# Performance work log

Hardware: AMD Instinct MI355X
Metric: run time of the kernel (lower is better)

## Reference

```python
import jax, jax.numpy as jnp
import numpy as np

N, D, B, E = 3072, 64, 12, 49152


def _gat_conv(x, mask, W, a_src, a_dst, b):
    # PyG GATConv (eval mode): per-edge score = LeakyReLU(a_dst.Wx_i + a_src.Wx_j),
    # softmax over incoming neighbors (mask includes self-loops), concat heads.
    H, d = a_src.shape
    h = (x @ W).reshape(x.shape[0], H, d)                  # [N, H, d]
    es = jnp.einsum('nhd,hd->nh', h, a_src)                # source-side score
    ed = jnp.einsum('nhd,hd->nh', h, a_dst)                # dest-side score
    e = jax.nn.leaky_relu(ed[:, None, :] + es[None, :, :], 0.2)  # [Ndst, Nsrc, H]
    e = jnp.where(mask[:, :, None], e, -jnp.inf)
    alpha = jax.nn.softmax(e, axis=1)                      # softmax over sources
    out = jnp.einsum('ijh,jhd->ihd', alpha, h)
    return out.reshape(x.shape[0], H * d) + b


def _gcn_conv(x, Abool, W, b):
    # PyG GCNConv: add self-loops, symmetric deg^{-1/2} normalization.
    n = x.shape[0]
    Ahat = Abool.astype(x.dtype) + jnp.eye(n, dtype=x.dtype)
    deg = Ahat.sum(1)
    dinv = jnp.where(deg > 0, 1.0 / jnp.sqrt(deg), 0.0)
    return (dinv[:, None] * Ahat * dinv[None, :]) @ (x @ W) + b


def _forward(x, ei, g1_W, g1_as, g1_ad, g1_b, g2_W, g2_as, g2_ad, g2_b,
             gA_W, gA_b, gB_W, gB_b, gC_W, gC_b, c2_W, c2_b, c3_W, c3_b,
             hwA_W, hwA_b, hwB_W, hwB_b, gru_Wih, gru_Whh, gru_bih, gru_bhh,
             tA_W, tA_b, tB_W, tB_b, edge_index, atom_list, res_list):
    n = x.shape[0]
    relu = jax.nn.relu
    I = jnp.eye(n, dtype=bool)
    # A[dst, src] = 1 (PyG messages flow src -> dst); ei only sets to_dense_adj
    # values in the original, which are never used (only adj.shape).
    A = jnp.zeros((n, n), dtype=bool).at[edge_index[1], edge_index[0]].set(True)
    Af = A.astype(x.dtype)
    A2 = (Af @ Af) > 0                      # spspmm(E, E): 2-hop edges
    A3 = (Af @ A2.astype(x.dtype)) > 0      # spspmm(E^2, E): 3-hop edges
    counts = atom_list + res_list
    batch = jnp.repeat(jnp.arange(counts.shape[0]), counts, total_repeat_length=n)

    def gat_block(mask):
        v = jax.nn.elu(_gat_conv(x, mask, g1_W, g1_as, g1_ad, g1_b))
        v = relu(_gat_conv(v, mask, g2_W, g2_as, g2_ad, g2_b))
        v = relu(v @ gA_W + gA_b)
        v = relu(v @ gB_W + gB_b)
        return v @ gC_W + gC_b

    h1 = relu(gat_block(A | I))
    h1 = relu(_gcn_conv(h1, A, c2_W, c2_b))
    h1 = relu(_gcn_conv(h1, A, c3_W, c3_b))          # [N, 4D]
    h2 = relu(gat_block(A2 | I))
    h2 = relu(_gcn_conv(h2, A2, c2_W, c2_b))          # [N, 2D]
    h3 = relu(gat_block(A3 | I))                      # [N, D]
    # HighWay fusion
    bb = h2 @ hwB_W + hwB_b
    aa = h1 @ hwA_W + hwA_b
    z = jax.nn.sigmoid(aa + bb)
    hh = z * bb + (1.0 - z) * aa
    # GRUCell(input=h3, hidden=hh), PyTorch gate order r, z, n
    gx = h3 @ gru_Wih + gru_bih
    gh = hh @ gru_Whh + gru_bhh
    xr, xz, xn = jnp.split(gx, 3, axis=1)
    hr, hz, hn = jnp.split(gh, 3, axis=1)
    r = jax.nn.sigmoid(xr + hr)
    zz = jax.nn.sigmoid(xz + hz)
    nn_ = jnp.tanh(xn + r * hn)
    cc = (1.0 - zz) * nn_ + zz * hh
    vi = jax.ops.segment_max(cc, batch, num_segments=atom_list.shape[0])  # global_max_pool
    vi = relu(vi @ tA_W + tA_b)
    return vi @ tB_W + tB_b


def setup_inputs() -> dict:
    key = jax.random.key(0)
    ks = jax.random.split(key, 40)
    it = iter(range(40))

    def p(shp):
        return jax.random.normal(ks[next(it)], shp, dtype=jnp.float32) * 0.1

    src = jax.random.randint(ks[next(it)], (E,), 0, N)
    dst = jax.random.randint(ks[next(it)], (E,), 0, N)
    dst = jnp.where(dst == src, (dst + 1) % N, dst)   # no self-loops in raw edges
    edge_index = jnp.stack([src, dst])
    inp = {
        'x': jax.random.normal(ks[next(it)], (N, D), dtype=jnp.float32),
        'ei': jax.random.uniform(ks[next(it)], (E,), dtype=jnp.float32),
        'g1_W': p((D, 8 * D)), 'g1_as': p((8, D)), 'g1_ad': p((8, D)), 'g1_b': p((8 * D,)),
        'g2_W': p((8 * D, D)), 'g2_as': p((1, D)), 'g2_ad': p((1, D)), 'g2_b': p((D,)),
        'gA_W': p((D, D)), 'gA_b': p((D,)), 'gB_W': p((D, 128)), 'gB_b': p((128,)),
        'gC_W': p((128, D)), 'gC_b': p((D,)),
        'c2_W': p((D, 2 * D)), 'c2_b': p((2 * D,)), 'c3_W': p((2 * D, 4 * D)), 'c3_b': p((4 * D,)),
        'hwA_W': p((4 * D, D)), 'hwA_b': p((D,)), 'hwB_W': p((2 * D, D)), 'hwB_b': p((D,)),
        'gru_Wih': p((D, 3 * D)), 'gru_Whh': p((D, 3 * D)), 'gru_bih': p((3 * D,)), 'gru_bhh': p((3 * D,)),
        'tA_W': p((D, 128)), 'tA_b': p((128,)), 'tB_W': p((128, 120)), 'tB_b': p((120,)),
        'edge_index': edge_index,
        'atom_list': jnp.full((B,), 156, dtype=jnp.int32),
        'res_list': jnp.full((B,), 100, dtype=jnp.int32),
    }
    return inp


def reference(x, ei, g1_W, g1_as, g1_ad, g1_b, g2_W, g2_as, g2_ad, g2_b,
              gA_W, gA_b, gB_W, gB_b, gC_W, gC_b, c2_W, c2_b, c3_W, c3_b,
              hwA_W, hwA_b, hwB_W, hwB_b, gru_Wih, gru_Whh, gru_bih, gru_bhh,
              tA_W, tA_b, tB_W, tB_b, edge_index, atom_list, res_list):
    return _forward(x, ei, g1_W, g1_as, g1_ad, g1_b, g2_W, g2_as, g2_ad, g2_b,
                    gA_W, gA_b, gB_W, gB_b, gC_W, gC_b, c2_W, c2_b, c3_W, c3_b,
                    hwA_W, hwA_b, hwB_W, hwB_b, gru_Wih, gru_Whh, gru_bih, gru_bhh,
                    tA_W, tA_b, tB_W, tB_b, edge_index, atom_list, res_list)
```

## Files before the change

### kernel.cpp

```cpp
#include <hip/hip_runtime.h>
#include <math.h>

namespace {

constexpr int NN = 3072;
constexpr int NW = 96;
constexpr int NEDGE_C = 49152;
constexpr int NB = 12;

using short8v = __attribute__((ext_vector_type(8))) short;
using f32x4v  = __attribute__((ext_vector_type(4))) float;
typedef unsigned short ushort_t;

__device__ __forceinline__ float leaky02(float x) { return x > 0.f ? x : 0.2f * x; }
__device__ __forceinline__ float sigm(float x) { return 1.f / (1.f + __expf(-x)); }

__device__ __forceinline__ ushort_t f2bf(float x) {
  unsigned u = __float_as_uint(x);
  return (ushort_t)((u + 0x7fffu + ((u >> 16) & 1u)) >> 16);
}
__device__ __forceinline__ float bf2f(ushort_t b) {
  return __uint_as_float(((unsigned)b) << 16);
}
__device__ __forceinline__ unsigned pack_h(float a, float b) {
  return (unsigned)f2bf(a) | ((unsigned)f2bf(b) << 16);
}
__device__ __forceinline__ unsigned pack_l(float a, float b) {
  float ra = a - bf2f(f2bf(a));
  float rb = b - bf2f(f2bf(b));
  return (unsigned)f2bf(ra) | ((unsigned)f2bf(rb) << 16);
}

template<int ACT> __device__ __forceinline__ float act_apply(float v) {
  if (ACT == 1) return fmaxf(v, 0.f);
  if (ACT == 2) return v > 0.f ? v : (__expf(v) - 1.f);
  return v;
}

__global__ __launch_bounds__(256) void k_scatter(const int* __restrict__ ei,
                                                 unsigned* __restrict__ bits) {
  int e = blockIdx.x * 256 + threadIdx.x;
  if (e < NEDGE_C) {
    int s = ei[e];
    int d = ei[NEDGE_C + e];
    atomicOr(&bits[(size_t)d * NW + (s >> 5)], 1u << (s & 31));
  }
}

__global__ __launch_bounds__(128) void k_bmm(const unsigned* __restrict__ a,
                                             const unsigned* __restrict__ src2,
                                             unsigned* __restrict__ outb) {
  __shared__ unsigned row[NW];
  int d = blockIdx.x;
  int t = threadIdx.x;
  if (t < NW) row[t] = a[(size_t)d * NW + t];
  __syncthreads();
  unsigned acc = 0;
  for (int w = 0; w < NW; ++w) {
    unsigned m = row[w];
    while (m) {
      int b = __ffs(m) - 1; m &= m - 1;
      int k = w * 32 + b;
      if (t < NW) acc |= src2[(size_t)k * NW + t];
    }
  }
  if (t < NW) outb[(size_t)d * NW + t] = acc;
}

__global__ __launch_bounds__(256) void k_dinv(const unsigned* __restrict__ bits,
                                              float* __restrict__ dinv) {
  int i = blockIdx.x * 256 + threadIdx.x;
  if (i < NN) {
    int c = 0;
    for (int w = 0; w < NW; ++w) c += __popc(bits[(size_t)i * NW + w]);
    dinv[i] = 1.0f / sqrtf((float)(c + 1));
  }
}

template<int ACT>
__global__ __launch_bounds__(256) void k_gemm(const float* __restrict__ X,
                                              const float* __restrict__ Wm,
                                              const float* __restrict__ bias,
                                              float* __restrict__ Y,
                                              int K, int Nc) {
  __shared__ float Xt[32][68];
  __shared__ float Wt[32][68];
  int R0 = blockIdx.x * 64, C0 = blockIdx.y * 64;
  int t = threadIdx.x;
  int rg = t >> 4, dg = t & 15;
  float acc[4][4] = {{0.f}};
  for (int k0 = 0; k0 < K; k0 += 32) {
    {
      int r = t >> 2, kq = (t & 3) * 8;
      const float* xp = X + (size_t)(R0 + r) * K + k0 + kq;
      float4 a0 = *(const float4*)xp;
      float4 a1 = *(const float4*)(xp + 4);
      Xt[kq + 0][r] = a0.x; Xt[kq + 1][r] = a0.y; Xt[kq + 2][r] = a0.z; Xt[kq + 3][r] = a0.w;
      Xt[kq + 4][r] = a1.x; Xt[kq + 5][r] = a1.y; Xt[kq + 6][r] = a1.z; Xt[kq + 7][r] = a1.w;
      int kk = t >> 3, cq = (t & 7) * 8;
      const float* wp = Wm + (size_t)(k0 + kk) * Nc + C0 + cq;
      *(float4*)&Wt[kk][cq]     = *(const float4*)wp;
      *(float4*)&Wt[kk][cq + 4] = *(const float4*)(wp + 4);
    }
    __syncthreads();
    #pragma unroll 8
    for (int k = 0; k < 32; ++k) {
      float4 av = *(const float4*)&Xt[k][rg * 4];
      float4 bv = *(const float4*)&Wt[k][dg * 4];
      float ar[4] = {av.x, av.y, av.z, av.w};
      float br[4] = {bv.x, bv.y, bv.z, bv.w};
      #pragma unroll
      for (int ri = 0; ri < 4; ++ri)
        #pragma unroll
        for (int ci = 0; ci < 4; ++ci)
          acc[ri][ci] += ar[ri] * br[ci];
    }
    __syncthreads();
  }
  float bv[4] = {0.f, 0.f, 0.f, 0.f};
  if (bias) {
    bv[0] = bias[C0 + dg * 4 + 0]; bv[1] = bias[C0 + dg * 4 + 1];
    bv[2] = bias[C0 + dg * 4 + 2]; bv[3] = bias[C0 + dg * 4 + 3];
  }
  for (int ri = 0; ri < 4; ++ri) {
    int row = R0 + rg * 4 + ri;
    float4 o;
    float* op = (float*)&o;
    #pragma unroll
    for (int ci = 0; ci < 4; ++ci)
      op[ci] = act_apply<ACT>(acc[ri][ci] + bv[ci]);
    *(float4*)&Y[(size_t)row * Nc + C0 + dg * 4] = o;
  }
}

template<int H>
__global__ __launch_bounds__(64) void k_scores(const float* __restrict__ h,
                                               const float* __restrict__ as,
                                               const float* __restrict__ ad,
                                               float* __restrict__ es,
                                               float* __restrict__ ed) {
  int i = blockIdx.x, lane = threadIdx.x;
  for (int hh = 0; hh < H; ++hh) {
    float v = h[(size_t)i * (H * 64) + hh * 64 + lane];
    float e1 = v * as[hh * 64 + lane];
    float e2 = v * ad[hh * 64 + lane];
    for (int off = 32; off > 0; off >>= 1) {
      e1 += __shfl_down(e1, off);
      e2 += __shfl_down(e2, off);
    }
    if (lane == 0) { es[(size_t)i * H + hh] = e1; ed[(size_t)i * H + hh] = e2; }
  }
}

__global__ __launch_bounds__(256) void k_gmax8(const float* __restrict__ es,
                                               float* __restrict__ gm) {
  __shared__ float sred[256 * 8];
  int t = threadIdx.x;
  float m[8];
  #pragma unroll
  for (int h = 0; h < 8; ++h) m[h] = -3.0e38f;
  for (int j = t; j < NN; j += 256) {
    float4 e0 = *(const float4*)&es[(size_t)j * 8];
    float4 e1 = *(const float4*)&es[(size_t)j * 8 + 4];
    m[0] = fmaxf(m[0], e0.x); m[1] = fmaxf(m[1], e0.y);
    m[2] = fmaxf(m[2], e0.z); m[3] = fmaxf(m[3], e0.w);
    m[4] = fmaxf(m[4], e1.x); m[5] = fmaxf(m[5], e1.y);
    m[6] = fmaxf(m[6], e1.z); m[7] = fmaxf(m[7], e1.w);
  }
  #pragma unroll
  for (int h = 0; h < 8; ++h) sred[t * 8 + h] = m[h];
  __syncthreads();
  for (int s = 128; s > 0; s >>= 1) {
    if (t < s) {
      #pragma unroll
      for (int h = 0; h < 8; ++h)
        sred[t * 8 + h] = fmaxf(sred[t * 8 + h], sred[(t + s) * 8 + h]);
    }
    __syncthreads();
  }
  if (t < 8) gm[t] = sred[t];
}

__global__ __launch_bounds__(256) void k_gmax1b(const float* __restrict__ es,
                                                float* __restrict__ gm) {
  __shared__ float red[256];
  int t = threadIdx.x;
  const float* e = es + (size_t)blockIdx.x * NN;
  float m = -3.0e38f;
  for (int j = t; j < NN; j += 256) m = fmaxf(m, e[j]);
  red[t] = m;
  __syncthreads();
  for (int s = 128; s > 0; s >>= 1) {
    if (t < s) red[t] = fmaxf(red[t], red[t + s]);
    __syncthreads();
  }
  if (t == 0) gm[blockIdx.x] = red[0];
}

__device__ __forceinline__ int enum_bits16(const unsigned* rowb, int p,
                                           unsigned* jlist, int* cnt, int t) {
  if (t < 16) {
    int base = 0;
    for (int k = 0; k < t; ++k) base += __popc(rowb[p * 16 + k]);
    unsigned m = rowb[p * 16 + t];
    int j0 = p * 512 + t * 32;
    while (m) { int b = __ffs(m) - 1; m &= m - 1; jlist[base++] = j0 + b; }
    if (t == 15) *cnt = base;
  }
  __syncthreads();
  return *cnt;
}

template<int ACT>
__global__ __launch_bounds__(256) void k_gat_sparse8(const float* __restrict__ hsrc,
                                                     const float* __restrict__ es,
                                                     const float* __restrict__ ed,
                                                     const float* __restrict__ gm,
                                                     const unsigned* __restrict__ bits,
                                                     const float* __restrict__ bias,
                                                     float* __restrict__ out) {
  __shared__ unsigned rowb[NW];
  __shared__ unsigned jlist[512];
  __shared__ float wl[512 * 8];
  __shared__ int cnt;
  __shared__ float red[256];
  __shared__ float sden[8];
  int i = blockIdx.x, t = threadIdx.x;
  if (t < NW) {
    unsigned wv_ = bits[(size_t)i * NW + t];
    if (t == (i >> 5)) wv_ |= 1u << (i & 31);
    rowb[t] = wv_;
  }
  int wv = t >> 6, lane = t & 63;
  int ha = lane >> 4;
  int hb = 4 + (lane >> 4);
  int ca = lane * 4;
  float4 a0 = {0.f, 0.f, 0.f, 0.f};
  float4 a1 = {0.f, 0.f, 0.f, 0.f};
  int hw = t & 7;
  float edv = ed[(size_t)i * 8 + hw];
  float mh = leaky02(edv + gm[hw]);
  float dloc = 0.f;
  __syncthreads();

  for (int p = 0; p < 6; ++p) {
    __syncthreads();
    int c = enum_bits16(rowb, p, jlist, &cnt, t);
    if (c == 0) continue;
    for (int pidx = t; pidx < c * 8; pidx += 256) {
      int idx = pidx >> 3;
      int j = (int)jlist[idx];
      float s = leaky02(edv + es[(size_t)j * 8 + hw]);
      float w = __expf(s - mh);
      wl[idx * 8 + hw] = w;
      dloc += w;
    }
    __syncthreads();
    int idx = wv;
    for (; idx + 4 < c; idx += 8) {
      int j0 = (int)jlist[idx], j1 = (int)jlist[idx + 4];
      float w0a = wl[idx * 8 + ha],     w0b = wl[idx * 8 + hb];
      float w1a = wl[(idx + 4) * 8 + ha], w1b = wl[(idx + 4) * 8 + hb];
      float4 u0 = *(const float4*)&hsrc[(size_t)j0 * 512 + ca];
      float4 u1 = *(const float4*)&hsrc[(size_t)j0 * 512 + 256 + ca];
      float4 v0 = *(const float4*)&hsrc[(size_t)j1 * 512 + ca];
      float4 v1 = *(const float4*)&hsrc[(size_t)j1 * 512 + 256 + ca];
      a0.x += w0a * u0.x; a0.y += w0a * u0.y; a0.z += w0a * u0.z; a0.w += w0a * u0.w;
      a1.x += w0b * u1.x; a1.y += w0b * u1.y; a1.z += w0b * u1.z; a1.w += w0b * u1.w;
      a0.x += w1a * v0.x; a0.y += w1a * v0.y; a0.z += w1a * v0.z; a0.w += w1a * v0.w;
      a1.x += w1b * v1.x; a1.y += w1b * v1.y; a1.z += w1b * v1.z; a1.w += w1b * v1.w;
    }
    if (idx < c) {
      int j0 = (int)jlist[idx];
      float w0a = wl[idx * 8 + ha], w0b = wl[idx * 8 + hb];
      float4 u0 = *(const float4*)&hsrc[(size_t)j0 * 512 + ca];
      float4 u1 = *(const float4*)&hsrc[(size_t)j0 * 512 + 256 + ca];
      a0.x += w0a * u0.x; a0.y += w0a * u0.y; a0.z += w0a * u0.z; a0.w += w0a * u0.w;
      a1.x += w0b * u1.x; a1.y += w0b * u1.y; a1.z += w0b * u1.z; a1.w += w0b * u1.w;
    }
  }
  __syncthreads();
  red[t] = dloc;
  float* rbuf = wl;
  *(float4*)&rbuf[wv * 512 + ca] = a0;
  *(float4*)&rbuf[wv * 512 + 256 + ca] = a1;
  __syncthreads();
  if (t < 8) {
    float s = 0.f;
    for (int k = t; k < 256; k += 8) s += red[k];
    sden[t] = s;
  }
  __syncthreads();
  int cc0 = 2 * t, h2 = cc0 >> 6;
  float inv = 1.0f / sden[h2];
  float s0 = rbuf[cc0] + rbuf[512 + cc0] + rbuf[1024 + cc0] + rbuf[1536 + cc0];
  float s1 = rbuf[cc0 + 1] + rbuf[512 + cc0 + 1] + rbuf[1024 + cc0 + 1] + rbuf[1536 + cc0 + 1];
  float2 o;
  o.x = act_apply<ACT>(s0 * inv + bias[cc0]);
  o.y = act_apply<ACT>(s1 * inv + bias[cc0 + 1]);
  *(float2*)&out[(size_t)i * 512 + cc0] = o;
}

template<int ACT>
__global__ __launch_bounds__(256) void k_gat_sparse1(const float* __restrict__ hsrc,
                                                     const float* __restrict__ es,
                                                     const float* __restrict__ ed,
                                                     const float* __restrict__ gm,
                                                     const unsigned* __restrict__ bits,
                                                     const float* __restrict__ bias,
                                                     float* __restrict__ out) {
  __shared__ unsigned rowb[NW];
  __shared__ unsigned jlist[512];
  __shared__ float wl[512];
  __shared__ int cnt;
  __shared__ float red[256];
  __shared__ float red2[16 * 64];
  int i = blockIdx.x, t = threadIdx.x;
  if (t < NW) {
    unsigned wv_ = bits[(size_t)i * NW + t];
    if (t == (i >> 5)) wv_ |= 1u << (i & 31);
    rowb[t] = wv_;
  }
  int wv = t >> 6, lane = t & 63;
  int sub = lane >> 4;
  int col4 = (lane & 15) * 4;
  int g = wv * 4 + sub;
  float4 a = {0.f, 0.f, 0.f, 0.f};
  float edv = ed[i];
  float mh = leaky02(edv + gm[0]);
  float dloc = 0.f;
  __syncthreads();

  for (int p = 0; p < 6; ++p) {
    __syncthreads();
    int c = enum_bits16(rowb, p, jlist, &cnt, t);
    if (c == 0) continue;
    for (int idx = t; idx < c; idx += 256) {
      int j = (int)jlist[idx];
      float s = leaky02(edv + es[j]);
      float w = __expf(s - mh);
      wl[idx] = w;
      dloc += w;
    }
    __syncthreads();
    for (int base = 0; base < c; base += 16) {
      int idx = base + g;
      if (idx < c) {
        int j = (int)jlist[idx];
        float w = wl[idx];
        float4 v = *(const float4*)&hsrc[(size_t)j * 64 + col4];
        a.x += w * v.x; a.y += w * v.y; a.z += w * v.z; a.w += w * v.w;
      }
    }
  }
  __syncthreads();
  red[t] = dloc;
  __syncthreads();
  for (int s = 128; s > 0; s >>= 1) {
    if (t < s) red[t] += red[t + s];
    __syncthreads();
  }
  float inv = 1.0f / red[0];
  *(float4*)&red2[g * 64 + col4] = a;
  __syncthreads();
  if (t < 64) {
    float s = 0.f;
    #pragma unroll
    for (int k = 0; k < 16; ++k) s += red2[k * 64 + t];
    out[(size_t)i * 64 + t] = act_apply<ACT>(s * inv + bias[t]);
  }
}

__global__ __launch_bounds__(256) void k_split_h(const float* __restrict__ hb, int CS,
                                                 ushort_t* __restrict__ hhT,
                                                 ushort_t* __restrict__ hlT) {
  __shared__ float T[64][65];
  int j0 = blockIdx.x * 64, hh = blockIdx.y;
  int t = threadIdx.x;
  int cb = (t & 15) * 4, jrow = t >> 4;
  #pragma unroll
  for (int p = 0; p < 4; ++p) {
    int j = jrow + 16 * p;
    float4 v = *(const float4*)&hb[(size_t)(j0 + j) * CS + hh * 64 + cb];
    T[j][cb] = v.x; T[j][cb + 1] = v.y; T[j][cb + 2] = v.z; T[j][cb + 3] = v.w;
  }
  __syncthreads();
  int c = t >> 2, jq = (t & 3) * 16;
  float x[16];
  #pragma unroll
  for (int k = 0; k < 16; ++k) x[k] = T[jq + k][c];
  size_t base = ((size_t)hh * 64 + c) * NN + j0 + jq;
  uint4 u;
  u.x = pack_h(x[0], x[1]);  u.y = pack_h(x[2], x[3]);
  u.z = pack_h(x[4], x[5]);  u.w = pack_h(x[6], x[7]);
  *(uint4*)&hhT[base] = u;
  u.x = pack_h(x[8], x[9]);  u.y = pack_h(x[10], x[11]);
  u.z = pack_h(x[12], x[13]); u.w = pack_h(x[14], x[15]);
  *(uint4*)&hhT[base + 8] = u;
  u.x = pack_l(x[0], x[1]);  u.y = pack_l(x[2], x[3]);
  u.z = pack_l(x[4], x[5]);  u.w = pack_l(x[6], x[7]);
  *(uint4*)&hlT[base] = u;
  u.x = pack_l(x[8], x[9]);  u.y = pack_l(x[10], x[11]);
  u.z = pack_l(x[12], x[13]); u.w = pack_l(x[14], x[15]);
  *(uint4*)&hlT[base + 8] = u;
}

template<int H, int JS>
__global__ __launch_bounds__(256) void k_gat_dense_mfma(
    const ushort_t* __restrict__ hhT,
    const ushort_t* __restrict__ hlT,
    const float* __restrict__ es,
    const float* __restrict__ ed,
    const float* __restrict__ gm,
    const unsigned* __restrict__ bits,
    float* __restrict__ pacc,
    float* __restrict__ pden) {
  constexpr int CS = H * 64;
  constexpr int TILES = (NN / 32) / JS;
  constexpr int LW = 40;
  __shared__ ushort_t WhS[64 * LW], WlS[64 * LW];
  __shared__ ushort_t BhS[64 * LW], BlS[64 * LW];
  __shared__ float est[32];
  __shared__ unsigned mword[64];
  __shared__ float edl[64], ml[64];
  __shared__ float sred[4][64];
  int R0 = blockIdx.x * 64, hh = blockIdx.y, z = blockIdx.z;
  int t = threadIdx.x;
  int rr = t & 63, jr = t >> 6;
  int wid = t >> 6, lane = t & 63;
  int arow = lane & 15, kg = lane >> 4;
  int sc = t >> 2, sjo = (t & 3) * 8;
  const ushort_t* hhp = hhT + ((size_t)hh * 64 + sc) * NN + sjo;
  const ushort_t* hlp = hlT + ((size_t)hh * 64 + sc) * NN + sjo;
  f32x4v acc[4];
  #pragma unroll
  for (int nf = 0; nf < 4; ++nf) acc[nf] = (f32x4v){0.f, 0.f, 0.f, 0.f};
  float spart = 0.f;
  if (t < 64) {
    float e = ed[(size_t)(R0 + t) * H + hh];
    edl[t] = e;
    ml[t] = leaky02(e + gm[hh]);
  }
  int aoff = (wid * 16 + arow) * LW + kg * 8;

  for (int tt = 0; tt < TILES; ++tt) {
    int tile = z * TILES + tt, j0 = tile * 32;
    __syncthreads();
    uint4 rbh = *(const uint4*)(hhp + j0);
    uint4 rbl = *(const uint4*)(hlp + j0);
    if (t < 32) est[t] = es[(size_t)(j0 + t) * H + hh];
    if (t >= 64 && t < 128) mword[t - 64] = bits[(size_t)(R0 + t - 64) * NW + tile];
    __syncthreads();
    *(uint4*)&BhS[sc * LW + sjo] = rbh;
    *(uint4*)&BlS[sc * LW + sjo] = rbl;
    {
      unsigned wbits = mword[rr];
      int selfj = (R0 + rr) - j0;
      if (selfj >= 0 && selfj < 32) wbits |= (1u << selfj);
      float edv = edl[rr], mv = ml[rr];
      float w[8];
      #pragma unroll
      for (int q = 0; q < 8; ++q) {
        int jj = jr * 8 + q;
        float v = 0.f;
        if (wbits & (1u << jj)) v = __expf(leaky02(edv + est[jj]) - mv);
        w[q] = v;
        spart += v;
      }
      uint4 uh, ul;
      uh.x = pack_h(w[0], w[1]); uh.y = pack_h(w[2], w[3]);
      uh.z = pack_h(w[4], w[5]); uh.w = pack_h(w[6], w[7]);
      ul.x = pack_l(w[0], w[1]); ul.y = pack_l(w[2], w[3]);
      ul.z = pack_l(w[4], w[5]); ul.w = pack_l(w[6], w[7]);
      *(uint4*)&WhS[rr * LW + jr * 8] = uh;
      *(uint4*)&WlS[rr * LW + jr * 8] = ul;
    }
    __syncthreads();
    short8v Ah = *(const short8v*)&WhS[aoff];
    short8v Al = *(const short8v*)&WlS[aoff];
    #pragma unroll
    for (int nf = 0; nf < 4; ++nf) {
      short8v bh = *(const short8v*)&BhS[(nf * 16 + arow) * LW + kg * 8];
      short8v bl = *(const short8v*)&BlS[(nf * 16 + arow) * LW + kg * 8];
      acc[nf] = __builtin_amdgcn_mfma_f32_16x16x32_bf16(Ah, bh, acc[nf], 0, 0, 0);
      acc[nf] = __builtin_amdgcn_mfma_f32_16x16x32_bf16(Ah, bl, acc[nf], 0, 0, 0);
      acc[nf] = __builtin_amdgcn_mfma_f32_16x16x32_bf16(Al, bh, acc[nf], 0, 0, 0);
    }
  }
  __syncthreads();
  sred[jr][rr] = spart;
  __syncthreads();
  if (t < 64)
    pden[((size_t)z * NN + R0 + t) * H + hh] =
        sred[0][t] + sred[1][t] + sred[2][t] + sred[3][t];
  #pragma unroll
  for (int nf = 0; nf < 4; ++nf) {
    #pragma unroll
    for (int r = 0; r < 4; ++r) {
      int row = R0 + wid * 16 + kg * 4 + r;
      int c = hh * 64 + nf * 16 + arow;
      pacc[((size_t)z * NN + row) * CS + c] = acc[nf][r];
    }
  }
}

template<int H, int ACT, int JS>
__global__ __launch_bounds__(256) void k_gat_dense_red(const float* __restrict__ pacc,
                                                       const float* __restrict__ pden,
                                                       const float* __restrict__ bias,
                                                       float* __restrict__ out) {
  constexpr int CS = H * 64;
  int idx = blockIdx.x * 256 + threadIdx.x;
  if (idx >= NN * CS) return;
  int row = idx / CS, c = idx - row * CS, hh = c >> 6;
  float a = 0.f, d = 0.f;
  #pragma unroll
  for (int z = 0; z < JS; ++z) a += pacc[((size_t)z * NN + row) * CS + c];
  #pragma unroll
  for (int z = 0; z < JS; ++z) d += pden[((size_t)z * NN + row) * H + hh];
  out[idx] = act_apply<ACT>(a / d + bias[c]);
}

template<int H, int ACT>
__global__ __launch_bounds__(256) void k_gat_dense(const float* __restrict__ hsrc,
                                                   const float* __restrict__ es,
                                                   const float* __restrict__ ed,
                                                   const float* __restrict__ gm,
                                                   const unsigned* __restrict__ bits,
                                                   const float* __restrict__ bias,
                                                   float* __restrict__ out) {
  constexpr int CS = H * 64;
  __shared__ float htile[32][68];
  __shared__ float wl[32][68];
  __shared__ float est[32];
  __shared__ unsigned mword[64];
  __shared__ float edl[64], ml[64];
  __shared__ float sred[4][64];
  int R0 = blockIdx.x * 64;
  int hh = blockIdx.y;
  int t = threadIdx.x;
  int rg = t >> 4, dg = t & 15;
  int rr = t & 63, jr = t >> 6;
  float acc[4][4] = {{0.f}};
  float spart = 0.f;
  if (t < 64) {
    float e = ed[(size_t)(R0 + t) * H + hh];
    edl[t] = e;
    ml[t] = leaky02(e + gm[hh]);
  }
  __syncthreads();
  for (int tile = 0; tile < NN / 32; ++tile) {
    int j0 = tile * 32;
    {
      int jj = t >> 3, cq = (t & 7) * 8;
      const float* hp = hsrc + (size_t)(j0 + jj) * CS + hh * 64 + cq;
      *(float4*)&htile[jj][cq]     = *(const float4*)hp;
      *(float4*)&htile[jj][cq + 4] = *(const float4*)(hp + 4);
    }
    if (t < 32) est[t] = es[(size_t)(j0 + t) * H + hh];
    if (t >= 64 && t < 128) mword[t - 64] = bits[(size_t)(R0 + t - 64) * NW + tile];
    __syncthreads();
    {
      unsigned wbits = mword[rr];
      int selfj = (R0 + rr) - j0;
      if (selfj >= 0 && selfj < 32) wbits |= (1u << selfj);
      float edv = edl[rr], mv = ml[rr];
      #pragma unroll
      for (int q = 0; q < 8; ++q) {
        int jj = (q << 2) | jr;
        float w = 0.f;
        if (wbits & (1u << jj)) {
          float s = leaky02(edv + est[jj]);
          w = __expf(s - mv);
        }
        wl[jj][rr] = w;
        spart += w;
      }
    }
    __syncthreads();
    #pragma unroll 8
    for (int jj = 0; jj < 32; ++jj) {
      float4 av = *(const float4*)&wl[jj][rg * 4];
      float4 bv = *(const float4*)&htile[jj][dg * 4];
      float ar[4] = {av.x, av.y, av.z, av.w};
      float br[4] = {bv.x, bv.y, bv.z, bv.w};
      #pragma unroll
      for (int ri = 0; ri < 4; ++ri)
        #pragma unroll
        for (int ci = 0; ci < 4; ++ci)
          acc[ri][ci] += ar[ri] * br[ci];
    }
    __syncthreads();
  }
  sred[jr][rr] = spart;
  __syncthreads();
  if (t < 64) ml[t] = sred[0][t] + sred[1][t] + sred[2][t] + sred[3][t];
  __syncthreads();
  int cbase = hh * 64 + dg * 4;
  float bv0 = bias[cbase], bv1 = bias[cbase + 1], bv2 = bias[cbase + 2], bv3 = bias[cbase + 3];
  for (int ri = 0; ri < 4; ++ri) {
    int r = rg * 4 + ri;
    float inv = 1.0f / ml[r];
    float4 o;
    o.x = act_apply<ACT>(acc[ri][0] * inv + bv0);
    o.y = act_apply<ACT>(acc[ri][1] * inv + bv1);
    o.z = act_apply<ACT>(acc[ri][2] * inv + bv2);
    o.w = act_apply<ACT>(acc[ri][3] * inv + bv3);
    *(float4*)&out[(size_t)(R0 + r) * CS + cbase] = o;
  }
}

__global__ __launch_bounds__(256) void k_gcn256(const float* __restrict__ xw,
                                                const unsigned* __restrict__ bits,
                                                const float* __restrict__ dinv,
                                                const float* __restrict__ bias,
                                                float* __restrict__ out) {
  __shared__ unsigned rowb[NW];
  __shared__ unsigned jlist[512];
  __shared__ int cnt;
  int i = blockIdx.x, t = threadIdx.x;
  if (t < NW) rowb[t] = bits[(size_t)i * NW + t];
  float acc = 0.f;
  __syncthreads();
  for (int p = 0; p < 6; ++p) {
    __syncthreads();
    int cN = enum_bits16(rowb, p, jlist, &cnt, t);
    for (int idx = 0; idx < cN; ++idx) {
      int j = (int)jlist[idx];
      acc += dinv[j] * xw[(size_t)j * 256 + t];
    }
  }
  float di = dinv[i];
  float v = di * (acc + di * xw[(size_t)i * 256 + t]) + bias[t];
  out[(size_t)i * 256 + t] = fmaxf(v, 0.f);
}

__global__ __launch_bounds__(256) void k_gcn128b(const float* __restrict__ xw,
                                                 const unsigned* __restrict__ b0,
                                                 const unsigned* __restrict__ b1,
                                                 const float* __restrict__ d0,
                                                 const float* __restrict__ d1,
                                                 const float* __restrict__ bias,
                                                 float* __restrict__ outb) {
  __shared__ unsigned rowb[NW];
  __shared__ unsigned jlist[512];
  __shared__ int cnt;
  __shared__ float red[256];
  int blk = blockIdx.x, t = threadIdx.x;
  int br = blk >= NN;
  int i = br ? blk - NN : blk;
  const unsigned* bits = br ? b1 : b0;
  const float* dinv = br ? d1 : d0;
  const float* xb = xw + (size_t)br * NN * 128;
  if (t < NW) rowb[t] = bits[(size_t)i * NW + t];
  int g = t >> 7, c = t & 127;
  float acc = 0.f;
  __syncthreads();
  for (int p = 0; p < 6; ++p) {
    __syncthreads();
    int cN = enum_bits16(rowb, p, jlist, &cnt, t);
    for (int idx = g; idx < cN; idx += 2) {
      int j = (int)jlist[idx];
      acc += dinv[j] * xb[(size_t)j * 128 + c];
    }
  }
  __syncthreads();
  red[t] = acc;
  __syncthreads();
  if (t < 128) {
    acc = red[t] + red[t + 128];
    float di = dinv[i];
    float v = di * (acc + di * xb[(size_t)i * 128 + c]) + bias[c];
    outb[(size_t)blk * 128 + c] = fmaxf(v, 0.f);
  }
}

__global__ __launch_bounds__(256) void k_highway(const float* __restrict__ aa,
                                                 const float* __restrict__ bb,
                                                 float* __restrict__ hh) {
  int idx = blockIdx.x * 256 + threadIdx.x;
  if (idx < NN * 64) {
    float a = aa[idx], b = bb[idx];
    float z = sigm(a + b);
    hh[idx] = z * b + (1.f - z) * a;
  }
}

__global__ __launch_bounds__(256) void k_gru(const float* __restrict__ gx,
                                             const float* __restrict__ gh,
                                             const float* __restrict__ hh,
                                             float* __restrict__ cc) {
  int idx = blockIdx.x * 256 + threadIdx.x;
  if (idx < NN * 64) {
    int i = idx >> 6, d = idx & 63;
    float xr = gx[(size_t)i * 192 + d];
    float xz = gx[(size_t)i * 192 + 64 + d];
    float xn = gx[(size_t)i * 192 + 128 + d];
    float hr = gh[(size_t)i * 192 + d];
    float hz = gh[(size_t)i * 192 + 64 + d];
    float hn = gh[(size_t)i * 192 + 128 + d];
    float r = sigm(xr + hr);
    float z = sigm(xz + hz);
    float n = tanhf(xn + r * hn);
    cc[idx] = (1.f - z) * n + z * hh[idx];
  }
}

__global__ __launch_bounds__(64) void k_pool(const float* __restrict__ cc,
                                             const int* __restrict__ atoms,
                                             const int* __restrict__ resl,
                                             float* __restrict__ vi) {
  int s = blockIdx.x, lane = threadIdx.x;
  int start = 0;
  for (int k = 0; k < s; ++k) start += atoms[k] + resl[k];
  int end = start + atoms[s] + resl[s];
  if (end > NN) end = NN;
  float m = -3.0e38f;
  for (int r = start; r < end; ++r) m = fmaxf(m, cc[(size_t)r * 64 + lane]);
  vi[s * 64 + lane] = m;
}

__global__ __launch_bounds__(256) void k_final(const float* __restrict__ vi,
                                               const float* __restrict__ tAW,
                                               const float* __restrict__ tAb,
                                               const float* __restrict__ tBW,
                                               const float* __restrict__ tBb,
                                               float* __restrict__ out) {
  __shared__ float v[NB * 64];
  __shared__ float t1[NB * 128];
  int t = threadIdx.x;
  for (int idx = t; idx < NB * 64; idx += 256) v[idx] = vi[idx];
  __syncthreads();
  for (int idx = t; idx < NB * 128; idx += 256) {
    int r = idx >> 7, c = idx & 127;
    float a = tAb[c];
    for (int k = 0; k < 64; ++k) a += v[r * 64 + k] * tAW[k * 128 + c];
    t1[idx] = fmaxf(a, 0.f);
  }
  __syncthreads();
  for (int idx = t; idx < NB * 120; idx += 256) {
    int r = idx / 120, c = idx % 120;
    float a = tBb[c];
    for (int k = 0; k < 128; ++k) a += t1[r * 128 + k] * tBW[k * 120 + c];
    out[idx] = a;
  }
}

}

extern "C" void kernel_launch(void* const* d_in, const int* in_sizes, int n_in,
                              void* d_out, int out_size, void* d_ws, size_t ws_size,
                              hipStream_t stream) {
  (void)in_sizes; (void)n_in; (void)out_size;
  const float* x     = (const float*)d_in[0];
  const float* g1_W  = (const float*)d_in[2];
  const float* g1_as = (const float*)d_in[3];
  const float* g1_ad = (const float*)d_in[4];
  const float* g1_b  = (const float*)d_in[5];
  const float* g2_W  = (const float*)d_in[6];
  const float* g2_as = (const float*)d_in[7];
  const float* g2_ad = (const float*)d_in[8];
  const float* g2_b  = (const float*)d_in[9];
  const float* gA_W  = (const float*)d_in[10];
  const float* gA_b  = (const float*)d_in[11];
  const float* gB_W  = (const float*)d_in[12];
  const float* gB_b  = (const float*)d_in[13];
  const float* gC_W  = (const float*)d_in[14];
  const float* gC_b  = (const float*)d_in[15];
  const float* c2_W  = (const float*)d_in[16];
  const float* c2_b  = (const float*)d_in[17];
  const float* c3_W  = (const float*)d_in[18];
  const float* c3_b  = (const float*)d_in[19];
  const float* hwA_W = (const float*)d_in[20];
  const float* hwA_b = (const float*)d_in[21];
  const float* hwB_W = (const float*)d_in[22];
  const float* hwB_b = (const float*)d_in[23];
  const float* gWih  = (const float*)d_in[24];
  const float* gWhh  = (const float*)d_in[25];
  const float* gbih  = (const float*)d_in[26];
  const float* gbhh  = (const float*)d_in[27];
  const float* tA_W  = (const float*)d_in[28];
  const float* tA_b  = (const float*)d_in[29];
  const float* tB_W  = (const float*)d_in[30];
  const float* tB_b  = (const float*)d_in[31];
  const int* edges   = (const int*)d_in[32];
  const int* atoms   = (const int*)d_in[33];
  const int* resl    = (const int*)d_in[34];
  float* out = (float*)d_out;

  unsigned* bitsA  = (unsigned*)d_ws;
  unsigned* bitsA2 = bitsA + (size_t)NN * NW;
  unsigned* bitsA3 = bitsA2 + (size_t)NN * NW;
  float* fp = (float*)(bitsA3 + (size_t)NN * NW);
  float* dinvA  = fp; fp += NN;
  float* dinvA2 = fp; fp += NN;
  float* HB     = fp; fp += (size_t)NN * 512;
  float* ES1    = fp; fp += (size_t)NN * 8;
  float* ED1    = fp; fp += (size_t)NN * 8;
  float* GM1    = fp; fp += 16;
  float* V1ALL  = fp; fp += (size_t)3 * NN * 512;
  float* H2BALL = fp; fp += (size_t)3 * NN * 64;
  float* ES2ALL = fp; fp += (size_t)3 * NN;
  float* ED2ALL = fp; fp += (size_t)3 * NN;
  float* GM2ALL = fp; fp += 16;
  float* V2ALL  = fp; fp += (size_t)3 * NN * 64;
  float* V3ALL  = fp; fp += (size_t)3 * NN * 64;
  float* V4ALL  = fp; fp += (size_t)3 * NN * 128;
  float* V5ALL  = fp; fp += (size_t)3 * NN * 64;
  float* XC2    = fp; fp += (size_t)2 * NN * 128;
  float* TG     = fp; fp += (size_t)2 * NN * 128;
  float* XC3    = fp; fp += (size_t)NN * 256;
  float* H1F    = fp; fp += (size_t)NN * 256;
  float* AAb    = fp; fp += (size_t)NN * 64;
  float* BBb    = fp; fp += (size_t)NN * 64;
  float* HHb    = fp; fp += (size_t)NN * 64;
  float* VI     = fp; fp += NB * 64;
  float* GX = V1ALL;
  float* GH = V1ALL + (size_t)NN * 192;
  float* CC = V1ALL + (size_t)NN * 384;
  char* cp = (char*)fp;
  ushort_t* HhT8 = (ushort_t*)cp; cp += (size_t)8 * 64 * NN * 2;
  ushort_t* HlT8 = (ushort_t*)cp; cp += (size_t)8 * 64 * NN * 2;
  ushort_t* HhT1 = (ushort_t*)cp; cp += (size_t)64 * NN * 2;
  ushort_t* HlT1 = (ushort_t*)cp; cp += (size_t)64 * NN * 2;
  float* PACC = (float*)cp; cp += (size_t)4 * NN * 512 * 4;
  float* PDEN = (float*)cp; cp += (size_t)16 * NN * 8 * 4;
  int mode = ((size_t)(cp - (char*)d_ws) <= ws_size) ? 1 : 0;

  float* H3F = V5ALL + (size_t)2 * NN * 64;
  float* H2F = TG + (size_t)NN * 128;

  hipMemsetAsync(bitsA, 0, (size_t)NN * NW * sizeof(unsigned), stream);
  k_scatter<<<(NEDGE_C + 255) / 256, 256, 0, stream>>>(edges, bitsA);
  k_bmm<<<NN, 128, 0, stream>>>(bitsA, bitsA, bitsA2);
  k_bmm<<<NN, 128, 0, stream>>>(bitsA, bitsA2, bitsA3);
  k_dinv<<<NN / 256, 256, 0, stream>>>(bitsA, dinvA);
  k_dinv<<<NN / 256, 256, 0, stream>>>(bitsA2, dinvA2);

  k_gemm<0><<<dim3(48, 8), 256, 0, stream>>>(x, g1_W, nullptr, HB, 64, 512);
  k_scores<8><<<NN, 64, 0, stream>>>(HB, g1_as, g1_ad, ES1, ED1);
  k_gmax8<<<1, 256, 0, stream>>>(ES1, GM1);

  k_gat_sparse8<2><<<NN, 256, 0, stream>>>(HB, ES1, ED1, GM1, bitsA, g1_b, V1ALL);
  k_gat_sparse8<2><<<NN, 256, 0, stream>>>(HB, ES1, ED1, GM1, bitsA2, g1_b, V1ALL + (size_t)NN * 512);
  if (mode) {
    k_split_h<<<dim3(48, 8), 256, 0, stream>>>(HB, 512, HhT8, HlT8);
    k_gat_dense_mfma<8, 4><<<dim3(48, 8, 4), 256, 0, stream>>>(HhT8, HlT8, ES1, ED1, GM1, bitsA3, PACC, PDEN);
    k_gat_dense_red<8, 2, 4><<<NN * 512 / 256, 256, 0, stream>>>(PACC, PDEN, g1_b, V1ALL + (size_t)2 * NN * 512);
  } else {
    k_gat_dense<8, 2><<<dim3(48, 8), 256, 0, stream>>>(HB, ES1, ED1, GM1, bitsA3, g1_b, V1ALL + (size_t)2 * NN * 512);
  }

  k_gemm<0><<<dim3(144, 1), 256, 0, stream>>>(V1ALL, g2_W, nullptr, H2BALL, 512, 64);
  k_scores<1><<<3 * NN, 64, 0, stream>>>(H2BALL, g2_as, g2_ad, ES2ALL, ED2ALL);
  k_gmax1b<<<3, 256, 0, stream>>>(ES2ALL, GM2ALL);

  k_gat_sparse1<1><<<NN, 256, 0, stream>>>(H2BALL, ES2ALL, ED2ALL, GM2ALL, bitsA, g2_b, V2ALL);
  k_gat_sparse1<1><<<NN, 256, 0, stream>>>(H2BALL + (size_t)NN * 64, ES2ALL + NN, ED2ALL + NN,
                                           GM2ALL + 1, bitsA2, g2_b, V2ALL + (size_t)NN * 64);
  if (mode) {
    k_split_h<<<dim3(48, 1), 256, 0, stream>>>(H2BALL + (size_t)2 * NN * 64, 64, HhT1, HlT1);
    k_gat_dense_mfma<1, 16><<<dim3(48, 1, 16), 256, 0, stream>>>(
        HhT1, HlT1, ES2ALL + 2 * NN, ED2ALL + 2 * NN, GM2ALL + 2, bitsA3, PACC, PDEN);
    k_gat_dense_red<1, 1, 16><<<NN * 64 / 256, 256, 0, stream>>>(PACC, PDEN, g2_b, V2ALL + (size_t)2 * NN * 64);
  } else {
    k_gat_dense<1, 1><<<dim3(48, 1), 256, 0, stream>>>(
        H2BALL + (size_t)2 * NN * 64, ES2ALL + 2 * NN, ED2ALL + 2 * NN, GM2ALL + 2, bitsA3, g2_b,
        V2ALL + (size_t)2 * NN * 64);
  }

  k_gemm<1><<<dim3(144, 1), 256, 0, stream>>>(V2ALL, gA_W, gA_b, V3ALL, 64, 64);
  k_gemm<1><<<dim3(144, 2), 256, 0, stream>>>(V3ALL, gB_W, gB_b, V4ALL, 64, 128);
  k_gemm<1><<<dim3(144, 1), 256, 0, stream>>>(V4ALL, gC_W, gC_b, V5ALL, 128, 64);

  k_gemm<0><<<dim3(96, 2), 256, 0, stream>>>(V5ALL, c2_W, nullptr, XC2, 64, 128);
  k_gcn128b<<<2 * NN, 256, 0, stream>>>(XC2, bitsA, bitsA2, dinvA, dinvA2, c2_b, TG);
  k_gemm<0><<<dim3(48, 4), 256, 0, stream>>>(TG, c3_W, nullptr, XC3, 128, 256);
  k_gcn256<<<NN, 256, 0, stream>>>(XC3, bitsA, dinvA, c3_b, H1F);

  k_gemm<0><<<dim3(48, 1), 256, 0, stream>>>(H1F, hwA_W, hwA_b, AAb, 256, 64);
  k_gemm<0><<<dim3(48, 1), 256, 0, stream>>>(H2F, hwB_W, hwB_b, BBb, 128, 64);
  k_highway<<<NN * 64 / 256, 256, 0, stream>>>(AAb, BBb, HHb);
  k_gemm<0><<<dim3(48, 3), 256, 0, stream>>>(H3F, gWih, gbih, GX, 64, 192);
  k_gemm<0><<<dim3(48, 3), 256, 0, stream>>>(HHb, gWhh, gbhh, GH, 64, 192);
  k_gru<<<NN * 64 / 256, 256, 0, stream>>>(GX, GH, HHb, CC);
  k_pool<<<NB, 64, 0, stream>>>(CC, atoms, resl, VI);
  k_final<<<1, 256, 0, stream>>>(VI, tA_W, tA_b, tB_W, tB_b, out);
}
```

Before: 607.0 us.

## Split sparse GAT over column partitions and run GCN aggregation with bf16 MFMA

Sparse GAT layer-1 aggregation is split into four column-range partitions per row, writing partial accumulators and denominators that the existing dense reduction kernel then combines. This raises parallelism over the one-block-per-row version. GCN layers drop the per-row sparse gather and instead compute a dense bitmask-times-features product on matrix cores. Features are pre-scaled by deg^-1/2 and split into hi/lo bf16 halves to keep near-fp32 accuracy, and the self-loop term is added in a separate reduction kernel. The cost is extra passes through the partial buffers in global memory and a dense product that spends work on zero entries of the adjacency.

```diff
diff --git a/kernel.cpp b/kernel.cpp
--- a/kernel.cpp
+++ b/kernel.cpp
@@ -211,6 +211,107 @@
   return *cnt;
 }
 
+template<int JS>
+__global__ __launch_bounds__(256) void k_gat_sparse8_part(
+    const float* __restrict__ hsrc,
+    const float* __restrict__ es,
+    const float* __restrict__ ed,
+    const float* __restrict__ gm,
+    const unsigned* __restrict__ bits,
+    float* __restrict__ pacc,
+    float* __restrict__ pden) {
+  constexpr int WPS = NW / JS;
+  constexpr int WPP = WPS / 2;
+  __shared__ unsigned rowb[WPS];
+  __shared__ unsigned jlist[WPP * 32];
+  __shared__ float wl[WPP * 32 * 8];
+  __shared__ int cnt;
+  __shared__ float red[256];
+  __shared__ float sden[8];
+  int i = blockIdx.x, z = blockIdx.y, t = threadIdx.x;
+  int w0 = z * WPS;
+  if (t < WPS) {
+    unsigned wv_ = bits[(size_t)i * NW + w0 + t];
+    if (w0 + t == (i >> 5)) wv_ |= 1u << (i & 31);
+    rowb[t] = wv_;
+  }
+  int wv = t >> 6, lane = t & 63;
+  int ha = lane >> 4;
+  int hb = 4 + (lane >> 4);
+  int ca = lane * 4;
+  float4 a0 = {0.f, 0.f, 0.f, 0.f};
+  float4 a1 = {0.f, 0.f, 0.f, 0.f};
+  int hw = t & 7;
+  float edv = ed[(size_t)i * 8 + hw];
+  float mh = leaky02(edv + gm[hw]);
+  float dloc = 0.f;
+  __syncthreads();
+
+  for (int p = 0; p < 2; ++p) {
+    __syncthreads();
+    if (t < WPP) {
+      int base = 0;
+      for (int k = p * WPP; k < p * WPP + t; ++k) base += __popc(rowb[k]);
+      unsigned m = rowb[p * WPP + t];
+      int j0 = (w0 + p * WPP + t) * 32;
+      while (m) { int b = __ffs(m) - 1; m &= m - 1; jlist[base++] = j0 + b; }
+      if (t == WPP - 1) cnt = base;
+    }
+    __syncthreads();
+    int c = cnt;
+    if (c == 0) continue;
+    for (int pidx = t; pidx < c * 8; pidx += 256) {
+      int idx = pidx >> 3;
+      int j = (int)jlist[idx];
+      float s = leaky02(edv + es[(size_t)j * 8 + hw]);
+      float w = __expf(s - mh);
+      wl[idx * 8 + hw] = w;
+      dloc += w;
+    }
+    __syncthreads();
+    int idx = wv;
+    for (; idx + 4 < c; idx += 8) {
+      int j0 = (int)jlist[idx], j1 = (int)jlist[idx + 4];
+      float w0a = wl[idx * 8 + ha],       w0b = wl[idx * 8 + hb];
+      float w1a = wl[(idx + 4) * 8 + ha], w1b = wl[(idx + 4) * 8 + hb];
+      float4 u0 = *(const float4*)&hsrc[(size_t)j0 * 512 + ca];
+      float4 u1 = *(const float4*)&hsrc[(size_t)j0 * 512 + 256 + ca];
+      float4 v0 = *(const float4*)&hsrc[(size_t)j1 * 512 + ca];
+      float4 v1 = *(const float4*)&hsrc[(size_t)j1 * 512 + 256 + ca];
+      a0.x += w0a * u0.x; a0.y += w0a * u0.y; a0.z += w0a * u0.z; a0.w += w0a * u0.w;
+      a1.x += w0b * u1.x; a1.y += w0b * u1.y; a1.z += w0b * u1.z; a1.w += w0b * u1.w;
+      a0.x += w1a * v0.x; a0.y += w1a * v0.y; a0.z += w1a * v0.z; a0.w += w1a * v0.w;
+      a1.x += w1b * v1.x; a1.y += w1b * v1.y; a1.z += w1b * v1.z; a1.w += w1b * v1.w;
+    }
+    if (idx < c) {
+      int j0 = (int)jlist[idx];
+      float w0a = wl[idx * 8 + ha], w0b = wl[idx * 8 + hb];
+      float4 u0 = *(const float4*)&hsrc[(size_t)j0 * 512 + ca];
+      float4 u1 = *(const float4*)&hsrc[(size_t)j0 * 512 + 256 + ca];
+      a0.x += w0a * u0.x; a0.y += w0a * u0.y; a0.z += w0a * u0.z; a0.w += w0a * u0.w;
+      a1.x += w0b * u1.x; a1.y += w0b * u1.y; a1.z += w0b * u1.z; a1.w += w0b * u1.w;
+    }
+  }
+  __syncthreads();
+  red[t] = dloc;
+  float* rbuf = wl;
+  *(float4*)&rbuf[wv * 512 + ca] = a0;
+  *(float4*)&rbuf[wv * 512 + 256 + ca] = a1;
+  __syncthreads();
+  if (t < 8) {
+    float s = 0.f;
+    for (int k = t; k < 256; k += 8) s += red[k];
+    pden[((size_t)z * NN + i) * 8 + t] = s;
+    sden[t] = s;
+  }
+  __syncthreads();
+  int cc0 = 2 * t;
+  float s0 = rbuf[cc0] + rbuf[512 + cc0] + rbuf[1024 + cc0] + rbuf[1536 + cc0];
+  float s1 = rbuf[cc0 + 1] + rbuf[512 + cc0 + 1] + rbuf[1024 + cc0 + 1] + rbuf[1536 + cc0 + 1];
+  float2 o; o.x = s0; o.y = s1;
+  *(float2*)&pacc[((size_t)z * NN + i) * 512 + cc0] = o;
+}
+
 template<int ACT>
 __global__ __launch_bounds__(256) void k_gat_sparse8(const float* __restrict__ hsrc,
                                                      const float* __restrict__ es,
@@ -259,7 +360,7 @@
     int idx = wv;
     for (; idx + 4 < c; idx += 8) {
       int j0 = (int)jlist[idx], j1 = (int)jlist[idx + 4];
-      float w0a = wl[idx * 8 + ha],     w0b = wl[idx * 8 + hb];
+      float w0a = wl[idx * 8 + ha],       w0b = wl[idx * 8 + hb];
       float w1a = wl[(idx + 4) * 8 + ha], w1b = wl[(idx + 4) * 8 + hb];
       float4 u0 = *(const float4*)&hsrc[(size_t)j0 * 512 + ca];
       float4 u1 = *(const float4*)&hsrc[(size_t)j0 * 512 + 256 + ca];
@@ -371,38 +472,40 @@
   }
 }
 
-__global__ __launch_bounds__(256) void k_split_h(const float* __restrict__ hb, int CS,
-                                                 ushort_t* __restrict__ hhT,
-                                                 ushort_t* __restrict__ hlT) {
+__global__ __launch_bounds__(256) void k_split_xws(const float* __restrict__ xw, int C,
+                                                   const float* __restrict__ dinv,
+                                                   ushort_t* __restrict__ hT,
+                                                   ushort_t* __restrict__ lT) {
   __shared__ float T[64][65];
-  int j0 = blockIdx.x * 64, hh = blockIdx.y;
+  int j0 = blockIdx.x * 64, cb0 = blockIdx.y * 64;
   int t = threadIdx.x;
   int cb = (t & 15) * 4, jrow = t >> 4;
   #pragma unroll
   for (int p = 0; p < 4; ++p) {
     int j = jrow + 16 * p;
-    float4 v = *(const float4*)&hb[(size_t)(j0 + j) * CS + hh * 64 + cb];
-    T[j][cb] = v.x; T[j][cb + 1] = v.y; T[j][cb + 2] = v.z; T[j][cb + 3] = v.w;
+    float dv = dinv ? dinv[j0 + j] : 1.f;
+    float4 v = *(const float4*)&xw[(size_t)(j0 + j) * C + cb0 + cb];
+    T[j][cb] = v.x * dv; T[j][cb + 1] = v.y * dv; T[j][cb + 2] = v.z * dv; T[j][cb + 3] = v.w * dv;
   }
   __syncthreads();
   int c = t >> 2, jq = (t & 3) * 16;
   float x[16];
   #pragma unroll
   for (int k = 0; k < 16; ++k) x[k] = T[jq + k][c];
-  size_t base = ((size_t)hh * 64 + c) * NN + j0 + jq;
+  size_t base = ((size_t)(cb0 + c)) * NN + j0 + jq;
   uint4 u;
   u.x = pack_h(x[0], x[1]);  u.y = pack_h(x[2], x[3]);
   u.z = pack_h(x[4], x[5]);  u.w = pack_h(x[6], x[7]);
-  *(uint4*)&hhT[base] = u;
+  *(uint4*)&hT[base] = u;
   u.x = pack_h(x[8], x[9]);  u.y = pack_h(x[10], x[11]);
   u.z = pack_h(x[12], x[13]); u.w = pack_h(x[14], x[15]);
-  *(uint4*)&hhT[base + 8] = u;
+  *(uint4*)&hT[base + 8] = u;
   u.x = pack_l(x[0], x[1]);  u.y = pack_l(x[2], x[3]);
   u.z = pack_l(x[4], x[5]);  u.w = pack_l(x[6], x[7]);
-  *(uint4*)&hlT[base] = u;
+  *(uint4*)&lT[base] = u;
   u.x = pack_l(x[8], x[9]);  u.y = pack_l(x[10], x[11]);
   u.z = pack_l(x[12], x[13]); u.w = pack_l(x[14], x[15]);
-  *(uint4*)&hlT[base + 8] = u;
+  *(uint4*)&lT[base + 8] = u;
 }
 
 template<int H, int JS>
@@ -608,6 +711,99 @@
     o.w = act_apply<ACT>(acc[ri][3] * inv + bv3);
     *(float4*)&out[(size_t)(R0 + r) * CS + cbase] = o;
   }
+}
+
+template<int JS>
+__global__ __launch_bounds__(256) void k_gcn_mfma(
+    const ushort_t* __restrict__ bhT,
+    const ushort_t* __restrict__ blT,
+    const unsigned* __restrict__ b0,
+    const unsigned* __restrict__ b1,
+    float* __restrict__ pacc,
+    int zRows, int rowOffY, int colOffY, int cStride) {
+  constexpr int TILES = (NN / 32) / JS;
+  constexpr int LW = 40;
+  __shared__ ushort_t BhS[128 * LW], BlS[128 * LW];
+  __shared__ unsigned mword[64];
+  int R0 = blockIdx.x * 64, y = blockIdx.y, z = blockIdx.z;
+  const unsigned* bits = y ? b1 : b0;
+  int t = threadIdx.x;
+  int wid = t >> 6, lane = t & 63;
+  int arow = lane & 15, kg = lane >> 4;
+  int sc = t >> 1, jh = (t & 1) * 16;
+  const ushort_t* bhp = bhT + ((size_t)y * 128 + sc) * NN + jh;
+  const ushort_t* blp = blT + ((size_t)y * 128 + sc) * NN + jh;
+  f32x4v acc[4][2];
+  #pragma unroll
+  for (int rf = 0; rf < 4; ++rf)
+    #pragma unroll
+    for (int cf = 0; cf < 2; ++cf) acc[rf][cf] = (f32x4v){0.f, 0.f, 0.f, 0.f};
+
+  for (int tt = 0; tt < TILES; ++tt) {
+    int tile = z * TILES + tt, j0 = tile * 32;
+    uint4 h0 = *(const uint4*)(bhp + j0);
+    uint4 h1 = *(const uint4*)(bhp + j0 + 8);
+    uint4 l0 = *(const uint4*)(blp + j0);
+    uint4 l1 = *(const uint4*)(blp + j0 + 8);
+    __syncthreads();
+    *(uint4*)&BhS[sc * LW + jh]     = h0;
+    *(uint4*)&BhS[sc * LW + jh + 8] = h1;
+    *(uint4*)&BlS[sc * LW + jh]     = l0;
+    *(uint4*)&BlS[sc * LW + jh + 8] = l1;
+    if (t < 64) mword[t] = bits[(size_t)(R0 + t) * NW + tile];
+    __syncthreads();
+    short8v Aw[4];
+    #pragma unroll
+    for (int rf = 0; rf < 4; ++rf) {
+      unsigned wb = mword[rf * 16 + arow];
+      unsigned oct = (wb >> (kg * 8)) & 0xffu;
+      #pragma unroll
+      for (int q = 0; q < 8; ++q)
+        Aw[rf][q] = (short)(((oct >> q) & 1u) ? 0x3f80 : 0);
+    }
+    #pragma unroll
+    for (int cf = 0; cf < 2; ++cf) {
+      int col = wid * 32 + cf * 16 + arow;
+      short8v bh = *(const short8v*)&BhS[col * LW + kg * 8];
+      short8v bl = *(const short8v*)&BlS[col * LW + kg * 8];
+      #pragma unroll
+      for (int rf = 0; rf < 4; ++rf) {
+        acc[rf][cf] = __builtin_amdgcn_mfma_f32_16x16x32_bf16(Aw[rf], bh, acc[rf][cf], 0, 0, 0);
+        acc[rf][cf] = __builtin_amdgcn_mfma_f32_16x16x32_bf16(Aw[rf], bl, acc[rf][cf], 0, 0, 0);
+      }
+    }
+  }
+  #pragma unroll
+  for (int rf = 0; rf < 4; ++rf)
+    #pragma unroll
+    for (int cf = 0; cf < 2; ++cf)
+      #pragma unroll
+      for (int r = 0; r < 4; ++r) {
+        int row = R0 + rf * 16 + kg * 4 + r;
+        int c = wid * 32 + cf * 16 + arow;
+        pacc[((size_t)z * zRows + (size_t)y * rowOffY + row) * cStride + y * colOffY + c] =
+            acc[rf][cf][r];
+      }
+}
+
+template<int JS>
+__global__ __launch_bounds__(256) void k_gcn_red(const float* __restrict__ pacc,
+                                                 const float* __restrict__ xw,
+                                                 const float* __restrict__ d0,
+                                                 const float* __restrict__ d1,
+                                                 const float* __restrict__ bias,
+                                                 float* __restrict__ out,
+                                                 int rowsTotal, int C) {
+  int idx = blockIdx.x * 256 + threadIdx.x;
+  if (idx >= rowsTotal * C) return;
+  int blk = idx / C, c = idx - blk * C;
+  float s = 0.f;
+  #pragma unroll
+  for (int z = 0; z < JS; ++z) s += pacc[((size_t)z * rowsTotal + blk) * C + c];
+  int i = blk >= NN ? blk - NN : blk;
+  float di = (blk >= NN ? d1 : d0)[i];
+  float v = di * (s + di * xw[(size_t)blk * C + c]) + bias[c];
+  out[idx] = fmaxf(v, 0.f);
 }
 
 __global__ __launch_bounds__(256) void k_gcn256(const float* __restrict__ xw,
@@ -819,10 +1015,12 @@
   float* GH = V1ALL + (size_t)NN * 192;
   float* CC = V1ALL + (size_t)NN * 384;
   char* cp = (char*)fp;
-  ushort_t* HhT8 = (ushort_t*)cp; cp += (size_t)8 * 64 * NN * 2;
-  ushort_t* HlT8 = (ushort_t*)cp; cp += (size_t)8 * 64 * NN * 2;
+  ushort_t* HhT8 = (ushort_t*)cp; cp += (size_t)512 * NN * 2;
+  ushort_t* HlT8 = (ushort_t*)cp; cp += (size_t)512 * NN * 2;
   ushort_t* HhT1 = (ushort_t*)cp; cp += (size_t)64 * NN * 2;
   ushort_t* HlT1 = (ushort_t*)cp; cp += (size_t)64 * NN * 2;
+  ushort_t* XWSH = (ushort_t*)cp; cp += (size_t)256 * NN * 2;
+  ushort_t* XWSL = (ushort_t*)cp; cp += (size_t)256 * NN * 2;
   float* PACC = (float*)cp; cp += (size_t)4 * NN * 512 * 4;
   float* PDEN = (float*)cp; cp += (size_t)16 * NN * 8 * 4;
   int mode = ((size_t)(cp - (char*)d_ws) <= ws_size) ? 1 : 0;
@@ -841,13 +1039,17 @@
   k_scores<8><<<NN, 64, 0, stream>>>(HB, g1_as, g1_ad, ES1, ED1);
   k_gmax8<<<1, 256, 0, stream>>>(ES1, GM1);
 
-  k_gat_sparse8<2><<<NN, 256, 0, stream>>>(HB, ES1, ED1, GM1, bitsA, g1_b, V1ALL);
-  k_gat_sparse8<2><<<NN, 256, 0, stream>>>(HB, ES1, ED1, GM1, bitsA2, g1_b, V1ALL + (size_t)NN * 512);
   if (mode) {
-    k_split_h<<<dim3(48, 8), 256, 0, stream>>>(HB, 512, HhT8, HlT8);
+    k_gat_sparse8_part<4><<<dim3(NN, 4), 256, 0, stream>>>(HB, ES1, ED1, GM1, bitsA, PACC, PDEN);
+    k_gat_dense_red<8, 2, 4><<<NN * 512 / 256, 256, 0, stream>>>(PACC, PDEN, g1_b, V1ALL);
+    k_gat_sparse8_part<4><<<dim3(NN, 4), 256, 0, stream>>>(HB, ES1, ED1, GM1, bitsA2, PACC, PDEN);
+    k_gat_dense_red<8, 2, 4><<<NN * 512 / 256, 256, 0, stream>>>(PACC, PDEN, g1_b, V1ALL + (size_t)NN * 512);
+    k_split_xws<<<dim3(48, 8), 256, 0, stream>>>(HB, 512, nullptr, HhT8, HlT8);
     k_gat_dense_mfma<8, 4><<<dim3(48, 8, 4), 256, 0, stream>>>(HhT8, HlT8, ES1, ED1, GM1, bitsA3, PACC, PDEN);
     k_gat_dense_red<8, 2, 4><<<NN * 512 / 256, 256, 0, stream>>>(PACC, PDEN, g1_b, V1ALL + (size_t)2 * NN * 512);
   } else {
+    k_gat_sparse8<2><<<NN, 256, 0, stream>>>(HB, ES1, ED1, GM1, bitsA, g1_b, V1ALL);
+    k_gat_sparse8<2><<<NN, 256, 0, stream>>>(HB, ES1, ED1, GM1, bitsA2, g1_b, V1ALL + (size_t)NN * 512);
     k_gat_dense<8, 2><<<dim3(48, 8), 256, 0, stream>>>(HB, ES1, ED1, GM1, bitsA3, g1_b, V1ALL + (size_t)2 * NN * 512);
   }
 
@@ -859,7 +1061,7 @@
   k_gat_sparse1<1><<<NN, 256, 0, stream>>>(H2BALL + (size_t)NN * 64, ES2ALL + NN, ED2ALL + NN,
                                            GM2ALL + 1, bitsA2, g2_b, V2ALL + (size_t)NN * 64);
   if (mode) {
-    k_split_h<<<dim3(48, 1), 256, 0, stream>>>(H2BALL + (size_t)2 * NN * 64, 64, HhT1, HlT1);
+    k_split_xws<<<dim3(48, 1), 256, 0, stream>>>(H2BALL + (size_t)2 * NN * 64, 64, nullptr, HhT1, HlT1);
     k_gat_dense_mfma<1, 16><<<dim3(48, 1, 16), 256, 0, stream>>>(
         HhT1, HlT1, ES2ALL + 2 * NN, ED2ALL + 2 * NN, GM2ALL + 2, bitsA3, PACC, PDEN);
     k_gat_dense_red<1, 1, 16><<<NN * 64 / 256, 256, 0, stream>>>(PACC, PDEN, g2_b, V2ALL + (size_t)2 * NN * 64);
@@ -874,9 +1076,23 @@
   k_gemm<1><<<dim3(144, 1), 256, 0, stream>>>(V4ALL, gC_W, gC_b, V5ALL, 128, 64);
 
   k_gemm<0><<<dim3(96, 2), 256, 0, stream>>>(V5ALL, c2_W, nullptr, XC2, 64, 128);
-  k_gcn128b<<<2 * NN, 256, 0, stream>>>(XC2, bitsA, bitsA2, dinvA, dinvA2, c2_b, TG);
+  if (mode) {
+    k_split_xws<<<dim3(48, 2), 256, 0, stream>>>(XC2, 128, dinvA, XWSH, XWSL);
+    k_split_xws<<<dim3(48, 2), 256, 0, stream>>>(XC2 + (size_t)NN * 128, 128, dinvA2,
+                                                 XWSH + (size_t)128 * NN, XWSL + (size_t)128 * NN);
+    k_gcn_mfma<8><<<dim3(48, 2, 8), 256, 0, stream>>>(XWSH, XWSL, bitsA, bitsA2, PACC, 2 * NN, NN, 0, 128);
+    k_gcn_red<8><<<2 * NN * 128 / 256, 256, 0, stream>>>(PACC, XC2, dinvA, dinvA2, c2_b, TG, 2 * NN, 128);
+  } else {
+    k_gcn128b<<<2 * NN, 256, 0, stream>>>(XC2, bitsA, bitsA2, dinvA, dinvA2, c2_b, TG);
+  }
   k_gemm<0><<<dim3(48, 4), 256, 0, stream>>>(TG, c3_W, nullptr, XC3, 128, 256);
-  k_gcn256<<<NN, 256, 0, stream>>>(XC3, bitsA, dinvA, c3_b, H1F);
+  if (mode) {
+    k_split_xws<<<dim3(48, 4), 256, 0, stream>>>(XC3, 256, dinvA, XWSH, XWSL);
+    k_gcn_mfma<8><<<dim3(48, 2, 8), 256, 0, stream>>>(XWSH, XWSL, bitsA, bitsA, PACC, NN, 0, 128, 256);
+    k_gcn_red<8><<<NN * 256 / 256, 256, 0, stream>>>(PACC, XC3, dinvA, dinvA, c3_b, H1F, NN, 256);
+  } else {
+    k_gcn256<<<NN, 256, 0, stream>>>(XC3, bitsA, dinvA, c3_b, H1F);
+  }
 
   k_gemm<0><<<dim3(48, 1), 256, 0, stream>>>(H1F, hwA_W, hwA_b, AAb, 256, 64);
   k_gemm<0><<<dim3(48, 1), 256, 0, stream>>>(H2F, hwB_W, hwB_b, BBb, 128, 64);
```

Result: faster. 585.8 us (-3.5%).
